# Kernel tuning notes

Measured on AMD Instinct MI355X. Metric: run time of the kernel, lower is better.

Reference implementation:

```python
import jax, jax.numpy as jnp
import numpy as np

N, E, G = 20000, 320000, 256
CAT, CONT, NEL = 16, 8, 9
HC, HE, HID, H, OUT = 32, 32, 64, 4, 128


def _gatv2(h, src, tgt, ee, Wl, bl, Wr, br, We, att, bias):
    # PyG GATv2Conv (eval mode, flow=source_to_target): messages aggregated at tgt
    n = h.shape[0]
    Hh, C = att.shape
    xl = (h @ Wl + bl).reshape(n, Hh, C)   # source transform
    xr = (h @ Wr + br).reshape(n, Hh, C)   # target transform
    ep = (ee @ We).reshape(-1, Hh, C)      # edge transform (no bias in PyG)
    m = jax.nn.leaky_relu(xl[src] + xr[tgt] + ep, 0.2)  # [E,H,C]
    e = jnp.einsum('ehc,hc->eh', m, att)                # [E,H]
    emax = jax.ops.segment_max(e, tgt, num_segments=n)
    p = jnp.exp(e - emax[tgt])
    denom = jax.ops.segment_sum(p, tgt, num_segments=n)
    alpha = p / (denom[tgt] + 1e-16)
    out = jax.ops.segment_sum(alpha[..., None] * xl[src], tgt, num_segments=n)
    return out.reshape(n, Hh * C) + bias


def setup_inputs() -> dict:
    key = jax.random.key(0)
    k = jax.random.split(key, 26)
    f = jnp.float32
    def w(kk, i, o):
        return jax.random.normal(kk, (i, o), f) / np.float32(np.sqrt(i))
    return {
        'x': jax.random.normal(k[0], (N, CAT + CONT), f),
        'edge_index': jax.random.randint(k[1], (2, E), 0, N, jnp.int32),
        'edge_attr': jax.random.uniform(k[2], (E, NEL), f),
        'batch': jnp.sort(jax.random.randint(k[3], (N,), 0, G, jnp.int32)),
        'W_cat': w(k[4], CAT, HC), 'b_cat': jnp.zeros((HC,), f),
        'W_e': w(k[5], NEL, HE), 'b_e': jnp.zeros((HE,), f),
        'W_init': w(k[6], CONT + HC, HID), 'b_init': jnp.zeros((HID,), f),
        'Wl1': w(k[7], HID, H * HID), 'bl1': jnp.zeros((H * HID,), f),
        'Wr1': w(k[8], HID, H * HID), 'br1': jnp.zeros((H * HID,), f),
        'We1': w(k[9], HE, H * HID),
        'att1': jax.random.normal(k[10], (H, HID), f) / np.float32(np.sqrt(HID)),
        'bias1': jnp.zeros((H * HID,), f),
        'Wl2': w(k[11], H * HID, HID), 'bl2': jnp.zeros((HID,), f),
        'Wr2': w(k[12], H * HID, HID), 'br2': jnp.zeros((HID,), f),
        'We2': w(k[13], HE, HID),
        'att2': jax.random.normal(k[14], (1, HID), f) / np.float32(np.sqrt(HID)),
        'bias2': jnp.zeros((HID,), f),
        'W_out': w(k[15], HID, OUT), 'b_out': jnp.zeros((OUT,), f),
    }


def reference(x, edge_index, edge_attr, batch,
              W_cat, b_cat, W_e, b_e, W_init, b_init,
              Wl1, bl1, Wr1, br1, We1, att1, bias1,
              Wl2, bl2, Wr2, br2, We2, att2, bias2,
              W_out, b_out):
    n = x.shape[0]
    f = x.dtype
    s = jax.nn.relu(x[:, :CAT] @ W_cat + b_cat)
    h = jnp.concatenate([x[:, CAT:], s], axis=1)
    h = jax.nn.relu(h @ W_init + b_init)
    ee = edge_attr @ W_e + b_e                       # [E, HE]
    src, tgt = edge_index[0], edge_index[1]
    # PyG GATv2Conv add_self_loops=True, fill_value='mean' on edge features
    cnt = jax.ops.segment_sum(jnp.ones((src.shape[0],), f), tgt, num_segments=n)
    loop_attr = jax.ops.segment_sum(ee, tgt, num_segments=n) / jnp.maximum(cnt, 1.0)[:, None]
    ar = jnp.arange(n, dtype=src.dtype)
    src2 = jnp.concatenate([src, ar])
    tgt2 = jnp.concatenate([tgt, ar])
    ee2 = jnp.concatenate([ee, loop_attr], axis=0)
    h = jax.nn.elu(_gatv2(h, src2, tgt2, ee2, Wl1, bl1, Wr1, br1, We1, att1, bias1))
    h = jax.nn.elu(_gatv2(h, src2, tgt2, ee2, Wl2, bl2, Wr2, br2, We2, att2, bias2))
    # global_mean_pool over graphs
    gcnt = jax.ops.segment_sum(jnp.ones((n,), f), batch, num_segments=G)
    pooled = jax.ops.segment_sum(h, batch, num_segments=G) / jnp.maximum(gcnt, 1.0)[:, None]
    return pooled @ W_out + b_out
```

## Files before the change

kernel.cpp:

```cpp
#include <hip/hip_runtime.h>
#include <hip/hip_bf16.h>

#define NN 20000
#define EE 320000
#define GG 256

__device__ __forceinline__ float lanebc(float v, int l){
  return __uint_as_float(__builtin_amdgcn_readlane(__float_as_uint(v), (unsigned)l));
}
__device__ __forceinline__ int lanebci(int v, int l){
  return __builtin_amdgcn_readlane(v, (unsigned)l);
}
__device__ __forceinline__ float wave_sum(float v){
  #pragma unroll
  for(int m=32;m>0;m>>=1) v += __shfl_xor(v, m, 64);
  return v;
}
__device__ __forceinline__ float wave_max(float v){
  #pragma unroll
  for(int m=32;m>0;m>>=1) v = fmaxf(v, __shfl_xor(v, m, 64));
  return v;
}
__device__ __forceinline__ float elu(float o){
  return (o > 0.f) ? o : (__expf(o) - 1.f);
}
__device__ __forceinline__ float bf2f(ushort u){ return __uint_as_float((unsigned)u << 16); }
__device__ __forceinline__ ushort f2bf(float f){
  unsigned x = __float_as_uint(f);
  return (ushort)((x + 0x7FFFu + ((x >> 16) & 1u)) >> 16);
}
__device__ __forceinline__ float2 up2(unsigned w){
  return make_float2(__uint_as_float(w << 16), __uint_as_float(w & 0xFFFF0000u));
}

template<int F>
__global__ void k_fold(const float* __restrict__ We9, const float* __restrict__ be,
                       const float* __restrict__ WeL, float* __restrict__ Wf, float* __restrict__ bf){
  const int c = threadIdx.x;
  #pragma unroll
  for (int j=0;j<9;j++){
    float a = 0.f;
    #pragma unroll
    for (int k=0;k<32;k++) a += We9[j*32+k]*WeL[k*F+c];
    Wf[j*F+c] = a;
  }
  float b = 0.f;
  #pragma unroll
  for (int k=0;k<32;k++) b += be[k]*WeL[k*F+c];
  bf[c] = b;
}

__global__ void k_node_mlp(const float* __restrict__ x, const float* __restrict__ Wcat,
                           const float* __restrict__ bcat, const float* __restrict__ Wini,
                           const float* __restrict__ bini, float* __restrict__ h0,
                           ushort* __restrict__ h0b){
  const int t = blockIdx.x;
  const int c = threadIdx.x;
  __shared__ float xs[24];
  __shared__ float s[32];
  if (c < 24) xs[c] = x[t*24 + c];
  __syncthreads();
  if (c < 32){
    float a = bcat[c];
    #pragma unroll
    for(int k=0;k<16;k++) a += xs[k]*Wcat[k*32 + c];
    s[c] = fmaxf(a, 0.f);
  }
  __syncthreads();
  float a = bini[c];
  #pragma unroll
  for(int k=0;k<8;k++)  a += xs[16+k]*Wini[k*64 + c];
  #pragma unroll
  for(int k=0;k<32;k++) a += s[k]*Wini[(8+k)*64 + c];
  const float r = fmaxf(a, 0.f);
  h0[t*64 + c] = r;
  h0b[t*64 + c] = f2bf(r);
}

__global__ void k_edge_acc(const int* __restrict__ ei, const float* __restrict__ ea,
                           float* __restrict__ loopA, int* __restrict__ cnt){
  const int g = blockIdx.x*16 + (threadIdx.x>>4);
  const int j = threadIdx.x & 15;
  if (g >= EE) return;
  const int t = ei[EE + g];
  if (j < 9)       atomicAdd(&loopA[t*12 + j], ea[(size_t)g*9 + j]);
  else if (j == 9) atomicAdd(&cnt[t], 1);
}

__global__ void k_alloc(const int* __restrict__ cnt, int* __restrict__ start, int* __restrict__ counter){
  int i = blockIdx.x*blockDim.x + threadIdx.x;
  if (i < NN) start[i] = atomicAdd(counter, cnt[i]);
}

__global__ void k_scatter(const int* __restrict__ ei, const int* __restrict__ start,
                          int* __restrict__ fill, int* __restrict__ csr,
                          int* __restrict__ srcp, int* __restrict__ tgtp){
  int e = blockIdx.x*blockDim.x + threadIdx.x;
  if (e >= EE) return;
  int t = ei[EE + e];
  int p = start[t] + atomicAdd(&fill[t], 1);
  csr[p] = e;
  srcp[p] = ei[e];
  tgtp[p] = t;
}

__global__ void k_xlxr1(const float* __restrict__ h0, const float* __restrict__ Wl,
                        const float* __restrict__ bl, const float* __restrict__ Wr,
                        const float* __restrict__ br, ushort* __restrict__ xl, ushort* __restrict__ xr){
  const int n0 = blockIdx.x*8;
  __shared__ __align__(16) float hsT[64][8];
  for(int i=threadIdx.x;i<512;i+=256){ int n=i>>6, k=i&63; hsT[k][n] = h0[(n0+n)*64 + k]; }
  __syncthreads();
  const int c = threadIdx.x;
  float accl[8], accr[8];
  const float blv = bl[c], brv = br[c];
  #pragma unroll
  for(int n=0;n<8;n++){ accl[n]=blv; accr[n]=brv; }
  for(int k=0;k<64;k++){
    const float wl = Wl[k*256 + c];
    const float wr = Wr[k*256 + c];
    const float4 ha = *(const float4*)&hsT[k][0];
    const float4 hb = *(const float4*)&hsT[k][4];
    accl[0]+=ha.x*wl; accr[0]+=ha.x*wr; accl[1]+=ha.y*wl; accr[1]+=ha.y*wr;
    accl[2]+=ha.z*wl; accr[2]+=ha.z*wr; accl[3]+=ha.w*wl; accr[3]+=ha.w*wr;
    accl[4]+=hb.x*wl; accr[4]+=hb.x*wr; accl[5]+=hb.y*wl; accr[5]+=hb.y*wr;
    accl[6]+=hb.z*wl; accr[6]+=hb.z*wr; accl[7]+=hb.w*wl; accr[7]+=hb.w*wr;
  }
  #pragma unroll
  for(int n=0;n<8;n++){
    xl[(size_t)(n0+n)*256 + c] = f2bf(accl[n]);
    xr[(size_t)(n0+n)*256 + c] = f2bf(accr[n]);
  }
}

template<int F>
__global__ __launch_bounds__(256) void k_score(const float* __restrict__ ea, const int* __restrict__ csr,
                        const int* __restrict__ srcp, const int* __restrict__ tgtp,
                        const ushort* __restrict__ xl, const ushort* __restrict__ xr,
                        const float* __restrict__ Wf, const float* __restrict__ bf,
                        const float* __restrict__ att, float* __restrict__ esc)
{
  constexpr int HP  = (F == 256) ? 2 : 1;
  constexpr int CPL = (F == 256) ? 8 : 4;
  const int tid  = threadIdx.x;
  const int lane = tid & 63;
  const int w    = tid >> 6;
  const int p0   = blockIdx.x * 64;

  __shared__ float ea_sT[9][64];
  __shared__ float Wf_s[9*F];
  __shared__ float bf_s[F];
  __shared__ int csr_s[64], src_s[64], tgt_s[64];

  if (tid < 64) { csr_s[tid] = csr[p0+tid]; src_s[tid] = srcp[p0+tid]; tgt_s[tid] = tgtp[p0+tid]; }
  __syncthreads();
  for (int i = tid; i < 576; i += 256){ int j = i>>6, ed = i&63; ea_sT[j][ed] = ea[(size_t)csr_s[ed]*9 + j]; }
  for (int i = tid; i < (9*F)/4; i += 256) ((float4*)Wf_s)[i] = ((const float4*)Wf)[i];
  if (tid < F) bf_s[tid] = bf[tid];
  __syncthreads();

  const int g = lane >> 4, t = lane & 15;
  const int eb = w*16 + g*4;

  #pragma unroll
  for (int hp = 0; hp < HP; ++hp) {
    const int c = hp*(F/HP) + t*CPL;
    float bfv[CPL];
    *(float4*)&bfv[0] = *(const float4*)&bf_s[c];
    if (CPL==8) *(float4*)&bfv[4] = *(const float4*)&bf_s[c+4];
    float acc[4][CPL];
    #pragma unroll
    for (int j=0;j<4;j++)
      #pragma unroll
      for(int q=0;q<CPL;q++) acc[j][q]=bfv[q];
    #pragma unroll
    for (int k=0;k<9;k++){
      const float4 ev = *(const float4*)&ea_sT[k][eb];
      float wv[CPL];
      *(float4*)&wv[0] = *(const float4*)&Wf_s[k*F + c];
      if (CPL==8) *(float4*)&wv[4] = *(const float4*)&Wf_s[k*F + c + 4];
      #pragma unroll
      for (int q=0;q<CPL;q++){
        acc[0][q] += ev.x*wv[q]; acc[1][q] += ev.y*wv[q];
        acc[2][q] += ev.z*wv[q]; acc[3][q] += ev.w*wv[q];
      }
    }
    float attv[CPL];
    *(float4*)&attv[0] = *(const float4*)&att[c];
    if (CPL==8) *(float4*)&attv[4] = *(const float4*)&att[c+4];
    float partial[4];
    #pragma unroll
    for (int j=0;j<4;j++){
      const int s  = src_s[eb+j];
      const int tg = tgt_s[eb+j];
      float xlv[CPL], xrv[CPL];
      if (CPL==8){
        const uint4 a = *(const uint4*)&xl[(size_t)s*F + c];
        const uint4 b = *(const uint4*)&xr[(size_t)tg*F + c];
        float2 p;
        p=up2(a.x); xlv[0]=p.x; xlv[1]=p.y;  p=up2(a.y); xlv[2]=p.x; xlv[3]=p.y;
        p=up2(a.z); xlv[4]=p.x; xlv[5]=p.y;  p=up2(a.w); xlv[6]=p.x; xlv[7]=p.y;
        p=up2(b.x); xrv[0]=p.x; xrv[1]=p.y;  p=up2(b.y); xrv[2]=p.x; xrv[3]=p.y;
        p=up2(b.z); xrv[4]=p.x; xrv[5]=p.y;  p=up2(b.w); xrv[6]=p.x; xrv[7]=p.y;
      } else {
        const uint2 a = *(const uint2*)&xl[(size_t)s*F + c];
        const uint2 b = *(const uint2*)&xr[(size_t)tg*F + c];
        float2 p;
        p=up2(a.x); xlv[0]=p.x; xlv[1]=p.y;  p=up2(a.y); xlv[2]=p.x; xlv[3]=p.y;
        p=up2(b.x); xrv[0]=p.x; xrv[1]=p.y;  p=up2(b.y); xrv[2]=p.x; xrv[3]=p.y;
      }
      float sum = 0.f;
      #pragma unroll
      for (int q=0;q<CPL;q++){
        float m = acc[j][q] + xlv[q] + xrv[q];
        m = (m >= 0.f) ? m : 0.2f*m;
        sum += attv[q]*m;
      }
      partial[j] = sum;
    }
    #pragma unroll
    for (int j=0;j<4;j++){
      partial[j] += __shfl_xor(partial[j], 1, 64);
      partial[j] += __shfl_xor(partial[j], 2, 64);
      partial[j] += __shfl_xor(partial[j], 4, 64);
      if (F==64) partial[j] += __shfl_xor(partial[j], 8, 64);
    }
    if (F==256){
      if ((t & 7) == 0){
        const int h = hp*2 + (t>>3);
        #pragma unroll
        for (int j=0;j<4;j++) esc[(size_t)h*EE + p0 + eb + j] = partial[j];
      }
    } else {
      if (t == 0){
        #pragma unroll
        for (int j=0;j<4;j++) esc[p0 + eb + j] = partial[j];
      }
    }
  }
}

__global__ __launch_bounds__(256) void k_agg1(
    const float* __restrict__ loopA, const int* __restrict__ cnt,
    const int* __restrict__ start, const int* __restrict__ srcp,
    const ushort* __restrict__ h0b, const ushort* __restrict__ xl, const ushort* __restrict__ xr,
    const float* __restrict__ Wf, const float* __restrict__ bf,
    const float* __restrict__ att, const float* __restrict__ esc,
    float* __restrict__ zb)
{
  const int t = blockIdx.x*4 + (threadIdx.x>>6);
  const int c = threadIdx.x & 63;
  const int st = start[t], dg = cnt[t];

  float epb[4];
  if (dg > 0){
    const float invc = 1.f/(float)dg;
    float la[9];
    #pragma unroll
    for (int j=0;j<9;j++) la[j] = loopA[t*12+j]*invc;
    #pragma unroll
    for (int hd=0;hd<4;hd++){
      float ep = bf[hd*64+c];
      #pragma unroll
      for (int j=0;j<9;j++) ep += la[j]*Wf[j*256 + hd*64 + c];
      epb[hd] = ep;
    }
  } else {
    #pragma unroll
    for (int hd=0;hd<4;hd++) epb[hd]=0.f;
  }
  const float h0t = bf2f(h0b[(size_t)t*64 + c]);
  float sSelf[4];
  #pragma unroll
  for (int hd=0;hd<4;hd++){
    float m = bf2f(xl[(size_t)t*256 + hd*64 + c]) + bf2f(xr[(size_t)t*256 + hd*64 + c]) + epb[hd];
    m = (m>=0.f)? m : 0.2f*m;
    sSelf[hd] = wave_sum(att[hd*64+c]*m);
  }

  int sL = 0;
  float escv[4];
  #pragma unroll
  for (int hd=0;hd<4;hd++) escv[hd] = -1e30f;
  if (c < dg){
    sL = srcp[st+c];
    #pragma unroll
    for (int hd=0;hd<4;hd++) escv[hd] = esc[(size_t)hd*EE + st + c];
  }
  float mx[4];
  #pragma unroll
  for (int hd=0;hd<4;hd++) mx[hd] = fmaxf(wave_max(escv[hd]), sSelf[hd]);
  for (int i=64;i<dg;i+=64){
    #pragma unroll
    for (int hd=0;hd<4;hd++){
      float v = (i+c<dg)? esc[(size_t)hd*EE + st+i+c] : -1e30f;
      mx[hd] = fmaxf(mx[hd], wave_max(v));
    }
  }
  float preg[4], den[4], z[4];
  #pragma unroll
  for (int hd=0;hd<4;hd++){
    preg[hd] = (c<dg)? __expf(escv[hd]-mx[hd]) : 0.f;
    const float pS = __expf(sSelf[hd]-mx[hd]);
    den[hd] = wave_sum(preg[hd]) + pS;
    z[hd] = pS*h0t;
  }
  const int d1 = min(dg,64);
  for (int i=0;i<d1;i+=4){
    const int s0=lanebci(sL,i), s1=lanebci(sL,i+1), s2=lanebci(sL,i+2), s3=lanebci(sL,i+3);
    const float v0=bf2f(h0b[(size_t)s0*64+c]), v1=bf2f(h0b[(size_t)s1*64+c]);
    const float v2=bf2f(h0b[(size_t)s2*64+c]), v3=bf2f(h0b[(size_t)s3*64+c]);
    #pragma unroll
    for (int hd=0;hd<4;hd++){
      z[hd] += lanebc(preg[hd],i)*v0;
      z[hd] += lanebc(preg[hd],i+1)*v1;
      z[hd] += lanebc(preg[hd],i+2)*v2;
      z[hd] += lanebc(preg[hd],i+3)*v3;
    }
  }
  for (int i=64;i<dg;i++){
    const float hv = bf2f(h0b[(size_t)srcp[st+i]*64+c]);
    #pragma unroll
    for (int hd=0;hd<4;hd++){
      const float pp = __expf(esc[(size_t)hd*EE+st+i]-mx[hd]);
      den[hd] += pp;
      z[hd] += pp*hv;
    }
  }
  #pragma unroll
  for (int hd=0;hd<4;hd++) zb[(size_t)t*256 + hd*64 + c] = z[hd]/(den[hd]+1e-16f);
}

__global__ __launch_bounds__(256) void k_h1xlxr2(
    const float* __restrict__ zb, const float* __restrict__ Wl1,
    const float* __restrict__ bl1, const float* __restrict__ bias1,
    const float* __restrict__ Wl2, const float* __restrict__ bl2,
    const float* __restrict__ Wr2, const float* __restrict__ br2,
    ushort* __restrict__ xl2, ushort* __restrict__ xr2)
{
  const int n0 = blockIdx.x*8;
  __shared__ __align__(16) float zT[256][8];
  __shared__ __align__(16) float hsT[256][8];
  const int tid = threadIdx.x;
  for (int i=tid;i<2048;i+=256){ int n=i>>8, k=i&255; zT[k][n] = zb[(size_t)(n0+n)*256 + k]; }
  __syncthreads();
  {
    const int c = tid, hd = tid>>6;
    float acc[8];
    const float b = bl1[c] + bias1[c];
    #pragma unroll
    for (int n=0;n<8;n++) acc[n]=b;
    #pragma unroll 2
    for (int k=0;k<64;k++){
      const float w = Wl1[k*256 + c];
      const float4 ha = *(const float4*)&zT[hd*64+k][0];
      const float4 hb = *(const float4*)&zT[hd*64+k][4];
      acc[0]+=ha.x*w; acc[1]+=ha.y*w; acc[2]+=ha.z*w; acc[3]+=ha.w*w;
      acc[4]+=hb.x*w; acc[5]+=hb.y*w; acc[6]+=hb.z*w; acc[7]+=hb.w*w;
    }
    #pragma unroll
    for (int n=0;n<8;n++) hsT[c][n] = elu(acc[n]);
  }
  __syncthreads();
  const int cc = tid & 63, ng = tid >> 6;
  float al0, al1, ar0, ar1;
  al0 = al1 = bl2[cc]; ar0 = ar1 = br2[cc];
  #pragma unroll 4
  for (int k=0;k<256;k++){
    const float wl = Wl2[k*64 + cc], wr = Wr2[k*64 + cc];
    const float2 hv = *(const float2*)&hsT[k][ng*2];
    al0 += hv.x*wl; ar0 += hv.x*wr; al1 += hv.y*wl; ar1 += hv.y*wr;
  }
  xl2[(size_t)(n0+ng*2  )*64 + cc] = f2bf(al0); xr2[(size_t)(n0+ng*2  )*64 + cc] = f2bf(ar0);
  xl2[(size_t)(n0+ng*2+1)*64 + cc] = f2bf(al1); xr2[(size_t)(n0+ng*2+1)*64 + cc] = f2bf(ar1);
}

__global__ __launch_bounds__(256) void k_agg2(
    const float* __restrict__ loopA, const int* __restrict__ cnt,
    const int* __restrict__ start, const int* __restrict__ srcp,
    const ushort* __restrict__ xl, const ushort* __restrict__ xr,
    const float* __restrict__ Wf, const float* __restrict__ bf,
    const float* __restrict__ att, const float* __restrict__ bias,
    const float* __restrict__ esc, float* __restrict__ hout)
{
  const int t = blockIdx.x*4 + (threadIdx.x>>6);
  const int c = threadIdx.x & 63;
  const int st = start[t], dg = cnt[t];

  float ep = 0.f;
  if (dg>0){
    const float invc = 1.f/(float)dg;
    ep = bf[c];
    #pragma unroll
    for (int j=0;j<9;j++) ep += (loopA[t*12+j]*invc)*Wf[j*64+c];
  }
  const float xlt = bf2f(xl[(size_t)t*64+c]);
  float m = xlt + bf2f(xr[(size_t)t*64+c]) + ep;
  m = (m>=0.f)? m : 0.2f*m;
  const float sSelf = wave_sum(att[c]*m);

  int sL=0; float escv=-1e30f;
  if (c<dg){ sL=srcp[st+c]; escv=esc[st+c]; }
  float mx = fmaxf(wave_max(escv), sSelf);
  for (int i=64;i<dg;i+=64){
    float v=(i+c<dg)? esc[st+i+c] : -1e30f;
    mx = fmaxf(mx, wave_max(v));
  }
  float preg = (c<dg)? __expf(escv-mx) : 0.f;
  const float pS = __expf(sSelf-mx);
  float den = wave_sum(preg)+pS;
  float z = pS*xlt;
  const int d1=min(dg,64);
  for (int i=0;i<d1;i+=4){
    const int s0=lanebci(sL,i),s1=lanebci(sL,i+1),s2=lanebci(sL,i+2),s3=lanebci(sL,i+3);
    const float p0=lanebc(preg,i),p1=lanebc(preg,i+1),p2=lanebc(preg,i+2),p3=lanebc(preg,i+3);
    const float v0=bf2f(xl[(size_t)s0*64+c]),v1=bf2f(xl[(size_t)s1*64+c]);
    const float v2=bf2f(xl[(size_t)s2*64+c]),v3=bf2f(xl[(size_t)s3*64+c]);
    z += p0*v0; z += p1*v1; z += p2*v2; z += p3*v3;
  }
  for (int i=64;i<dg;i++){
    const float pp=__expf(esc[st+i]-mx); den+=pp;
    z += pp*bf2f(xl[(size_t)srcp[st+i]*64+c]);
  }
  const float o = z/(den+1e-16f)+bias[c];
  hout[(size_t)t*64+c] = elu(o);
}

__global__ void k_pool(const float* __restrict__ h2, const int* __restrict__ batch,
                       float* __restrict__ pooled, int* __restrict__ gcnt){
  int i = blockIdx.x*blockDim.x + threadIdx.x;
  if (i >= NN*64) return;
  int node = i >> 6, c = i & 63;
  int g = batch[node];
  atomicAdd(&pooled[g*64 + c], h2[i]);
  if (c == 0) atomicAdd(&gcnt[g], 1);
}

__global__ void k_out(const float* __restrict__ pooled, const int* __restrict__ gcnt,
                      const float* __restrict__ Wout, const float* __restrict__ bout,
                      float* __restrict__ out){
  int g = blockIdx.x, o = threadIdx.x;
  float a = 0.f;
  for(int k=0;k<64;k++) a += pooled[g*64 + k] * Wout[k*128 + o];
  float inv = 1.f / fmaxf((float)gcnt[g], 1.f);
  out[g*128 + o] = a*inv + bout[o];
}

extern "C" void kernel_launch(void* const* d_in, const int* in_sizes, int n_in,
                              void* d_out, int out_size, void* d_ws, size_t ws_size,
                              hipStream_t stream) {
  const float* x    = (const float*)d_in[0];
  const int*   ei   = (const int*)  d_in[1];
  const float* ea   = (const float*)d_in[2];
  const int*   batch= (const int*)  d_in[3];
  const float* Wcat = (const float*)d_in[4];
  const float* bcat = (const float*)d_in[5];
  const float* We   = (const float*)d_in[6];
  const float* be   = (const float*)d_in[7];
  const float* Wini = (const float*)d_in[8];
  const float* bini = (const float*)d_in[9];
  const float* Wl1  = (const float*)d_in[10];
  const float* bl1  = (const float*)d_in[11];
  const float* Wr1  = (const float*)d_in[12];
  const float* br1  = (const float*)d_in[13];
  const float* We1  = (const float*)d_in[14];
  const float* att1 = (const float*)d_in[15];
  const float* bias1= (const float*)d_in[16];
  const float* Wl2  = (const float*)d_in[17];
  const float* bl2  = (const float*)d_in[18];
  const float* Wr2  = (const float*)d_in[19];
  const float* br2  = (const float*)d_in[20];
  const float* We2  = (const float*)d_in[21];
  const float* att2 = (const float*)d_in[22];
  const float* bias2= (const float*)d_in[23];
  const float* Wout = (const float*)d_in[24];
  const float* bout = (const float*)d_in[25];
  float* out = (float*)d_out;
  char* ws = (char*)d_ws;

  size_t off = 0;
  auto alloc = [&](size_t bytes)->char*{ char* p = ws + off; off += (bytes + 255) & ~(size_t)255; return p; };
  float*  h0    = (float*) alloc((size_t)NN*64*4);
  ushort* h0b   = (ushort*)alloc((size_t)NN*64*2);
  float*  loopA = (float*) alloc((size_t)NN*12*4);
  ushort* xl1   = (ushort*)alloc((size_t)NN*256*2);
  ushort* xr1   = (ushort*)alloc((size_t)NN*256*2);
  float*  zb    = (float*) alloc((size_t)NN*256*4);
  ushort* xl2   = (ushort*)alloc((size_t)NN*64*2);
  ushort* xr2   = (ushort*)alloc((size_t)NN*64*2);
  float*  h2    = (float*) alloc((size_t)NN*64*4);
  float*  esc   = (float*) alloc((size_t)EE*4*4);
  float*  Wf1   = (float*) alloc((size_t)9*256*4);
  float*  bf1   = (float*) alloc((size_t)256*4);
  float*  Wf2   = (float*) alloc((size_t)9*64*4);
  float*  bf2   = (float*) alloc((size_t)64*4);
  int*    cnt   = (int*)   alloc((size_t)NN*4);
  int*    start = (int*)   alloc((size_t)NN*4);
  int*    fill  = (int*)   alloc((size_t)NN*4);
  int*    csr   = (int*)   alloc((size_t)EE*4);
  int*    srcp  = (int*)   alloc((size_t)EE*4);
  int*    tgtp  = (int*)   alloc((size_t)EE*4);
  int*    counter = (int*) alloc(256);
  float*  pooled  = (float*)alloc((size_t)GG*64*4);
  int*    gcnt    = (int*)  alloc((size_t)GG*4);

  hipMemsetAsync(loopA,   0, (size_t)NN*12*4, stream);
  hipMemsetAsync(cnt,     0, (size_t)NN*4,    stream);
  hipMemsetAsync(fill,    0, (size_t)NN*4,    stream);
  hipMemsetAsync(counter, 0, 256,             stream);
  hipMemsetAsync(pooled,  0, (size_t)GG*64*4, stream);
  hipMemsetAsync(gcnt,    0, (size_t)GG*4,    stream);

  k_fold<256><<<1, 256, 0, stream>>>(We, be, We1, Wf1, bf1);
  k_fold<64> <<<1, 64, 0, stream>>>(We, be, We2, Wf2, bf2);
  k_node_mlp <<<NN, 64, 0, stream>>>(x, Wcat, bcat, Wini, bini, h0, h0b);
  k_edge_acc <<<EE/16, 256, 0, stream>>>(ei, ea, loopA, cnt);
  k_alloc    <<<(NN+255)/256, 256, 0, stream>>>(cnt, start, counter);
  k_scatter  <<<(EE+255)/256, 256, 0, stream>>>(ei, start, fill, csr, srcp, tgtp);
  k_xlxr1    <<<NN/8, 256, 0, stream>>>(h0, Wl1, bl1, Wr1, br1, xl1, xr1);
  k_score<256><<<EE/64, 256, 0, stream>>>(ea, csr, srcp, tgtp, xl1, xr1, Wf1, bf1, att1, esc);
  k_agg1     <<<NN/4, 256, 0, stream>>>(loopA, cnt, start, srcp, h0b, xl1, xr1, Wf1, bf1, att1, esc, zb);
  k_h1xlxr2  <<<NN/8, 256, 0, stream>>>(zb, Wl1, bl1, bias1, Wl2, bl2, Wr2, br2, xl2, xr2);
  k_score<64><<<EE/64, 256, 0, stream>>>(ea, csr, srcp, tgtp, xl2, xr2, Wf2, bf2, att2, esc);
  k_agg2     <<<NN/4, 256, 0, stream>>>(loopA, cnt, start, srcp, xl2, xr2, Wf2, bf2, att2, bias2, esc, h2);
  k_pool     <<<(NN*64+255)/256, 256, 0, stream>>>(h2, batch, pooled, gcnt);
  k_out      <<<GG, 128, 0, stream>>>(pooled, gcnt, Wout, bout, out);
}
```

Before: 357.9 us.

## Repack layer-2 weights as float4 and tile 16 nodes per block in h1xlxr2

Adds a prep kernel that repacks Wl1, Wl2 and Wr2 into k-interleaved float4 layouts. The fused layer-1 finish and layer-2 projection kernel now handles 16 nodes per block instead of 8, and uses padded shared-memory tiles. This is meant to halve weight re-reads per node and use wider vector loads. In exchange it adds an extra small kernel launch, more registers per thread, and half as many blocks.

```diff
diff --git a/kernel.cpp b/kernel.cpp
--- a/kernel.cpp
+++ b/kernel.cpp
@@ -48,6 +48,26 @@
   #pragma unroll
   for (int k=0;k<32;k++) b += be[k]*WeL[k*F+c];
   bf[c] = b;
+}
+
+__global__ void k_prep(const float* __restrict__ Wl1, const float* __restrict__ Wl2,
+                       const float* __restrict__ Wr2, float4* __restrict__ Wl1p4,
+                       float4* __restrict__ Wl2p4, float4* __restrict__ Wr2p4){
+  const int idx = (blockIdx.x%16)*256 + threadIdx.x;
+  const int seg = blockIdx.x/16;
+  if (seg == 0){
+    const int k4 = idx>>8, c = idx&255;
+    Wl1p4[idx] = make_float4(Wl1[(4*k4+0)*256+c], Wl1[(4*k4+1)*256+c],
+                             Wl1[(4*k4+2)*256+c], Wl1[(4*k4+3)*256+c]);
+  } else if (seg == 1){
+    const int k4 = idx>>6, cc = idx&63;
+    Wl2p4[idx] = make_float4(Wl2[(4*k4+0)*64+cc], Wl2[(4*k4+1)*64+cc],
+                             Wl2[(4*k4+2)*64+cc], Wl2[(4*k4+3)*64+cc]);
+  } else {
+    const int k4 = idx>>6, cc = idx&63;
+    Wr2p4[idx] = make_float4(Wr2[(4*k4+0)*64+cc], Wr2[(4*k4+1)*64+cc],
+                             Wr2[(4*k4+2)*64+cc], Wr2[(4*k4+3)*64+cc]);
+  }
 }
 
 __global__ void k_node_mlp(const float* __restrict__ x, const float* __restrict__ Wcat,
@@ -332,47 +352,71 @@
 }
 
 __global__ __launch_bounds__(256) void k_h1xlxr2(
-    const float* __restrict__ zb, const float* __restrict__ Wl1,
+    const float* __restrict__ zb, const float4* __restrict__ Wl1p4,
     const float* __restrict__ bl1, const float* __restrict__ bias1,
-    const float* __restrict__ Wl2, const float* __restrict__ bl2,
-    const float* __restrict__ Wr2, const float* __restrict__ br2,
+    const float4* __restrict__ Wl2p4, const float* __restrict__ bl2,
+    const float4* __restrict__ Wr2p4, const float* __restrict__ br2,
     ushort* __restrict__ xl2, ushort* __restrict__ xr2)
 {
-  const int n0 = blockIdx.x*8;
-  __shared__ __align__(16) float zT[256][8];
-  __shared__ __align__(16) float hsT[256][8];
+  const int n0 = blockIdx.x*16;
   const int tid = threadIdx.x;
-  for (int i=tid;i<2048;i+=256){ int n=i>>8, k=i&255; zT[k][n] = zb[(size_t)(n0+n)*256 + k]; }
+  __shared__ float zT[256*20];
+  __shared__ __align__(16) float4 hs[64][17];
+  #pragma unroll
+  for (int j=0;j<16;j++) zT[tid*20 + j] = zb[(size_t)(n0+j)*256 + tid];
   __syncthreads();
   {
-    const int c = tid, hd = tid>>6;
-    float acc[8];
+    const int c = tid, hd = c>>6;
+    float acc[16];
     const float b = bl1[c] + bias1[c];
     #pragma unroll
-    for (int n=0;n<8;n++) acc[n]=b;
-    #pragma unroll 2
-    for (int k=0;k<64;k++){
-      const float w = Wl1[k*256 + c];
-      const float4 ha = *(const float4*)&zT[hd*64+k][0];
-      const float4 hb = *(const float4*)&zT[hd*64+k][4];
-      acc[0]+=ha.x*w; acc[1]+=ha.y*w; acc[2]+=ha.z*w; acc[3]+=ha.w*w;
-      acc[4]+=hb.x*w; acc[5]+=hb.y*w; acc[6]+=hb.z*w; acc[7]+=hb.w*w;
-    }
-    #pragma unroll
-    for (int n=0;n<8;n++) hsT[c][n] = elu(acc[n]);
-  }
-  __syncthreads();
-  const int cc = tid & 63, ng = tid >> 6;
-  float al0, al1, ar0, ar1;
-  al0 = al1 = bl2[cc]; ar0 = ar1 = br2[cc];
-  #pragma unroll 4
-  for (int k=0;k<256;k++){
-    const float wl = Wl2[k*64 + cc], wr = Wr2[k*64 + cc];
-    const float2 hv = *(const float2*)&hsT[k][ng*2];
-    al0 += hv.x*wl; ar0 += hv.x*wr; al1 += hv.y*wl; ar1 += hv.y*wr;
-  }
-  xl2[(size_t)(n0+ng*2  )*64 + cc] = f2bf(al0); xr2[(size_t)(n0+ng*2  )*64 + cc] = f2bf(ar0);
-  xl2[(size_t)(n0+ng*2+1)*64 + cc] = f2bf(al1); xr2[(size_t)(n0+ng*2+1)*64 + cc] = f2bf(ar1);
+    for (int n=0;n<16;n++) acc[n]=b;
+    #pragma unroll 4
+    for (int k4=0;k4<16;k4++){
+      const float4 w4 = Wl1p4[k4*256 + c];
+      #pragma unroll
+      for (int kk=0;kk<4;kk++){
+        const float wk = (kk==0)?w4.x:(kk==1)?w4.y:(kk==2)?w4.z:w4.w;
+        const float* zr = &zT[(hd*64 + k4*4 + kk)*20];
+        const float4 z0 = *(const float4*)&zr[0];
+        const float4 z1 = *(const float4*)&zr[4];
+        const float4 z2 = *(const float4*)&zr[8];
+        const float4 z3 = *(const float4*)&zr[12];
+        acc[0]+=z0.x*wk; acc[1]+=z0.y*wk; acc[2]+=z0.z*wk; acc[3]+=z0.w*wk;
+        acc[4]+=z1.x*wk; acc[5]+=z1.y*wk; acc[6]+=z1.z*wk; acc[7]+=z1.w*wk;
+        acc[8]+=z2.x*wk; acc[9]+=z2.y*wk; acc[10]+=z2.z*wk; acc[11]+=z2.w*wk;
+        acc[12]+=z3.x*wk; acc[13]+=z3.y*wk; acc[14]+=z3.z*wk; acc[15]+=z3.w*wk;
+      }
+    }
+    float* hsf = (float*)hs;
+    const int base = (c>>2)*17*4 + (c&3);
+    #pragma unroll
+    for (int n=0;n<16;n++) hsf[base + n*4] = elu(acc[n]);
+  }
+  __syncthreads();
+  {
+    const int cc = tid & 63, ng = tid >> 6;
+    float al[4], ar[4];
+    const float bl = bl2[cc], br = br2[cc];
+    #pragma unroll
+    for (int j=0;j<4;j++){ al[j]=bl; ar[j]=br; }
+    #pragma unroll 4
+    for (int k4=0;k4<64;k4++){
+      const float4 wl = Wl2p4[k4*64 + cc];
+      const float4 wr = Wr2p4[k4*64 + cc];
+      #pragma unroll
+      for (int j=0;j<4;j++){
+        const float4 hv = hs[k4][ng*4 + j];
+        al[j] += hv.x*wl.x + hv.y*wl.y + hv.z*wl.z + hv.w*wl.w;
+        ar[j] += hv.x*wr.x + hv.y*wr.y + hv.z*wr.z + hv.w*wr.w;
+      }
+    }
+    #pragma unroll
+    for (int j=0;j<4;j++){
+      xl2[(size_t)(n0+ng*4+j)*64 + cc] = f2bf(al[j]);
+      xr2[(size_t)(n0+ng*4+j)*64 + cc] = f2bf(ar[j]);
+    }
+  }
 }
 
 __global__ __launch_bounds__(256) void k_agg2(
@@ -494,6 +538,9 @@
   float*  bf1   = (float*) alloc((size_t)256*4);
   float*  Wf2   = (float*) alloc((size_t)9*64*4);
   float*  bf2   = (float*) alloc((size_t)64*4);
+  float4* Wl1p4 = (float4*)alloc((size_t)4096*16);
+  float4* Wl2p4 = (float4*)alloc((size_t)4096*16);
+  float4* Wr2p4 = (float4*)alloc((size_t)4096*16);
   int*    cnt   = (int*)   alloc((size_t)NN*4);
   int*    start = (int*)   alloc((size_t)NN*4);
   int*    fill  = (int*)   alloc((size_t)NN*4);
@@ -513,6 +560,7 @@
 
   k_fold<256><<<1, 256, 0, stream>>>(We, be, We1, Wf1, bf1);
   k_fold<64> <<<1, 64, 0, stream>>>(We, be, We2, Wf2, bf2);
+  k_prep     <<<48, 256, 0, stream>>>(Wl1, Wl2, Wr2, Wl1p4, Wl2p4, Wr2p4);
   k_node_mlp <<<NN, 64, 0, stream>>>(x, Wcat, bcat, Wini, bini, h0, h0b);
   k_edge_acc <<<EE/16, 256, 0, stream>>>(ei, ea, loopA, cnt);
   k_alloc    <<<(NN+255)/256, 256, 0, stream>>>(cnt, start, counter);
@@ -520,7 +568,7 @@
   k_xlxr1    <<<NN/8, 256, 0, stream>>>(h0, Wl1, bl1, Wr1, br1, xl1, xr1);
   k_score<256><<<EE/64, 256, 0, stream>>>(ea, csr, srcp, tgtp, xl1, xr1, Wf1, bf1, att1, esc);
   k_agg1     <<<NN/4, 256, 0, stream>>>(loopA, cnt, start, srcp, h0b, xl1, xr1, Wf1, bf1, att1, esc, zb);
-  k_h1xlxr2  <<<NN/8, 256, 0, stream>>>(zb, Wl1, bl1, bias1, Wl2, bl2, Wr2, br2, xl2, xr2);
+  k_h1xlxr2  <<<NN/16, 256, 0, stream>>>(zb, Wl1p4, bl1, bias1, Wl2p4, bl2, Wr2p4, br2, xl2, xr2);
   k_score<64><<<EE/64, 256, 0, stream>>>(ea, csr, srcp, tgtp, xl2, xr2, Wf2, bf2, att2, esc);
   k_agg2     <<<NN/4, 256, 0, stream>>>(loopA, cnt, start, srcp, xl2, xr2, Wf2, bf2, att2, bias2, esc, h2);
   k_pool     <<<(NN*64+255)/256, 256, 0, stream>>>(h2, batch, pooled, gcnt);
```

After: 339.5 us. 1.05x faster.
